# Kernel tuning notes

Hardware: AMD Instinct MI355X
Metric: run time of the kernel (lower is better)

## Reference

```python
import jax, jax.numpy as jnp
import numpy as np

N = 131072      # points (rays x samples chunk)
E = 8           # spatial sub-networks (centroids)
DIN = 90        # encoded pos+dir features fed to sub-NeRFs (xyz_real=True -> x[:, 3:])
H = 256         # sub-NeRF hidden width
DOUT = 4        # rgb + sigma
MARGIN = 2.0    # boundary_margin
EPS = 1e-8


def setup_inputs() -> dict:
    key = jax.random.key(0)
    k = jax.random.split(key, 5)
    x_xyz = jax.random.uniform(k[0], (N, 3), dtype=jnp.float32)          # routing coords in [0,1)^3
    x_feat = jax.random.normal(k[1], (N, DIN), dtype=jnp.float32)        # encoded features
    x = jnp.concatenate([x_xyz, x_feat], axis=1)                         # [N, 3+DIN]
    centroids = jax.random.uniform(k[2], (E, 3), dtype=jnp.float32)
    W1 = jax.random.normal(k[3], (E, DIN, H), dtype=jnp.float32) * 0.05
    b1 = jnp.zeros((E, H), dtype=jnp.float32)
    W2 = jax.random.normal(k[4], (E, H, DOUT), dtype=jnp.float32) * 0.05
    b2 = jnp.zeros((E, DOUT), dtype=jnp.float32)
    return {"x": x, "centroids": centroids, "W1": W1, "b1": b1, "W2": W2, "b2": b2}


def reference(x, centroids, W1, b1, W2, b2):
    # --- centroid routing (torch.cdist equivalent) ---
    xyz = x[:, :3]                                                       # [N,3]
    d2 = jnp.sum((xyz[:, None, :] - centroids[None, :, :]) ** 2, axis=-1)
    dist = jnp.sqrt(jnp.maximum(d2, 0.0))                                # [N,E]
    inv = 1.0 / (dist + EPS)
    min_d = jnp.min(dist, axis=1, keepdims=True)                         # [N,1]
    inv = jnp.where(dist > MARGIN * min_d, 0.0, inv)                     # zero far experts
    weights = inv / jnp.sum(inv, axis=-1, keepdims=True)                 # [N,E], rows sum to 1

    # --- per-expert sub-NeRF MLP, weighted combine ---
    # Dense-equivalent of masked gather + weighted scatter-add: experts whose
    # weight is exactly 0 contribute nothing, matching the torch masked path.
    feat = x[:, 3:]                                                      # xyz_real=True -> drop xyz
    h = jax.nn.relu(jnp.einsum('nd,edh->enh', feat, W1) + b1[:, None, :])  # [E,N,H]
    out_e = jnp.einsum('enh,eho->eno', h, W2) + b2[:, None, :]             # [E,N,DOUT]
    return jnp.einsum('eno,ne->no', out_e, weights)                        # [N,DOUT]
```

## Files before the change

kernel.cpp:

```cpp
#include <hip/hip_runtime.h>

#define NPTS 131072
#define NE 8
#define DIN 90
#define NH 256
#define HPITCH 264

typedef __attribute__((ext_vector_type(8))) short bf16x8;
typedef __attribute__((ext_vector_type(4))) float f32x4;
typedef __attribute__((ext_vector_type(2))) float f32x2;
typedef __attribute__((ext_vector_type(4))) unsigned int u32x4;
typedef __attribute__((ext_vector_type(2))) unsigned int u32x2;
typedef __attribute__((ext_vector_type(4), aligned(4))) float f32x4a;
typedef __attribute__((ext_vector_type(2), aligned(4))) float f32x2a;

__device__ __forceinline__ unsigned short f2bf(float f) {
  unsigned int u = __float_as_uint(f);
  u += 0x7fffu + ((u >> 16) & 1u);
  return (unsigned short)(u >> 16);
}

__device__ __forceinline__ unsigned int pkbf(float f0, float f1) {
  unsigned int u0 = __float_as_uint(f0) + 0x7fffu;
  unsigned int u1 = __float_as_uint(f1) + 0x7fffu;
  return __builtin_amdgcn_perm(u1, u0, 0x07060302u);
}

__device__ __forceinline__ bf16x8 cvt8(f32x4 a, f32x4 b) {
  u32x4 r;
  r[0] = pkbf(a[0], a[1]);
  r[1] = pkbf(a[2], a[3]);
  r[2] = pkbf(b[0], b[1]);
  r[3] = pkbf(b[2], b[3]);
  return __builtin_bit_cast(bf16x8, r);
}

__global__ __launch_bounds__(256) void prep(const float* __restrict__ W1,
                                            const float* __restrict__ W2,
                                            unsigned short* __restrict__ W1T,
                                            unsigned short* __restrict__ W2T) {
  int idx = blockIdx.x * 256 + threadIdx.x;
  const int n1 = NE * NH * 96;
  if (idx < n1) {
    int kp = idx % 96;
    int n  = (idx / 96) % NH;
    int e  = idx / (96 * NH);
    float v = (kp < DIN) ? W1[((size_t)e * DIN + kp) * NH + n] : 0.f;
    W1T[idx] = f2bf(v);
  } else {
    int j = idx - n1;
    if (j < NE * 16 * NH) {
      int k = j % NH;
      int o = (j / NH) % 16;
      int e = j / (16 * NH);
      float v = (o < 4) ? W2[((size_t)e * NH + k) * 4 + o] : 0.f;
      W2T[j] = f2bf(v);
    }
  }
}

__global__ __launch_bounds__(256, 3) void meganerf_main(
    const float* __restrict__ x, const float* __restrict__ cent,
    const float* __restrict__ b1, const float* __restrict__ b2,
    const unsigned short* __restrict__ W1T, const unsigned short* __restrict__ W2T,
    float* __restrict__ out) {
  __shared__ unsigned short sH[64 * HPITCH];
  __shared__ float sW[NE][64];
  __shared__ float sB2[64][4];

  const int t    = threadIdx.x;
  const int lane = t & 63;
  const int wid  = t >> 6;
  const int l15  = lane & 15;
  const int l4   = lane >> 4;
  const int row0 = blockIdx.x * 64;

  bf16x8 bfr[4][3];
#pragma unroll
  for (int nf = 0; nf < 4; ++nf) {
    const float* gr = x + (size_t)(row0 + 16 * nf + l15) * 93 + 3;
    f32x4 v0, v1;
    v0 = *(const f32x4a*)(gr + 8 * l4);
    v1 = *(const f32x4a*)(gr + 8 * l4 + 4);
    bfr[nf][0] = cvt8(v0, v1);
    v0 = *(const f32x4a*)(gr + 32 + 8 * l4);
    v1 = *(const f32x4a*)(gr + 36 + 8 * l4);
    bfr[nf][1] = cvt8(v0, v1);
    if (l4 < 3) {
      v0 = *(const f32x4a*)(gr + 64 + 8 * l4);
      v1 = *(const f32x4a*)(gr + 68 + 8 * l4);
    } else {
      f32x2 tl = *(const f32x2a*)(gr + 88);
      v0[0] = tl[0]; v0[1] = tl[1]; v0[2] = 0.f; v0[3] = 0.f;
      v1[0] = 0.f; v1[1] = 0.f; v1[2] = 0.f; v1[3] = 0.f;
    }
    bfr[nf][2] = cvt8(v0, v1);
  }

  if (t < 64) {
    const float* gx = x + (size_t)(row0 + t) * 93;
    float px = gx[0], py = gx[1], pz = gx[2];
    float dist[NE], inv[NE];
    float mind = 3.4e38f;
#pragma unroll
    for (int e = 0; e < NE; ++e) {
      float dx = px - cent[e * 3 + 0];
      float dy = py - cent[e * 3 + 1];
      float dz = pz - cent[e * 3 + 2];
      float d2 = dx * dx + dy * dy + dz * dz;
      float d = sqrtf(fmaxf(d2, 0.f));
      dist[e] = d;
      inv[e] = 1.f / (d + 1e-8f);
      mind = fminf(mind, d);
    }
    float s = 0.f;
#pragma unroll
    for (int e = 0; e < NE; ++e) {
      if (dist[e] > 2.0f * mind) inv[e] = 0.f;
      s += inv[e];
    }
    float rs = 1.f / s;
    float bb[4] = {0.f, 0.f, 0.f, 0.f};
#pragma unroll
    for (int e = 0; e < NE; ++e) {
      float w = inv[e] * rs;
      sW[e][t] = w;
#pragma unroll
      for (int o = 0; o < 4; ++o) bb[o] += w * b2[e * 4 + o];
    }
#pragma unroll
    for (int o = 0; o < 4; ++o) sB2[t][o] = bb[o];
  }
  __syncthreads();

  f32x4 facc[4] = {{0.f, 0.f, 0.f, 0.f}, {0.f, 0.f, 0.f, 0.f},
                   {0.f, 0.f, 0.f, 0.f}, {0.f, 0.f, 0.f, 0.f}};

  for (int e = 0; e < NE; ++e) {
    float wv[4];
#pragma unroll
    for (int nf = 0; nf < 4; ++nf) wv[nf] = sW[e][16 * nf + l15];

#pragma unroll
    for (int c = 0; c < 2; ++c) {
      const int colbase = 128 * c + 32 * wid;
      f32x4 b1v[2];
#pragma unroll
      for (int mf = 0; mf < 2; ++mf)
        b1v[mf] = *(const f32x4*)(b1 + e * NH + colbase + 16 * mf + 4 * l4);
      f32x4 acc[2][4];
#pragma unroll
      for (int mf = 0; mf < 2; ++mf)
#pragma unroll
        for (int nf = 0; nf < 4; ++nf) acc[mf][nf] = b1v[mf];
#pragma unroll
      for (int ks = 0; ks < 3; ++ks) {
        bf16x8 w1f[2];
#pragma unroll
        for (int mf = 0; mf < 2; ++mf)
          w1f[mf] = *(const bf16x8*)(W1T +
              (size_t)(e * NH + colbase + 16 * mf + l15) * 96 + 32 * ks + 8 * l4);
#pragma unroll
        for (int mf = 0; mf < 2; ++mf)
#pragma unroll
          for (int nf = 0; nf < 4; ++nf)
            acc[mf][nf] = __builtin_amdgcn_mfma_f32_16x16x32_bf16(
                w1f[mf], bfr[nf][ks], acc[mf][nf], 0, 0, 0);
      }
#pragma unroll
      for (int mf = 0; mf < 2; ++mf) {
        const int hcol = colbase + 16 * mf + 4 * l4;
#pragma unroll
        for (int nf = 0; nf < 4; ++nf) {
          const float w = wv[nf];
          f32x4 a = acc[mf][nf];
          f32x2 p0, p1;
          p0[0] = a[0]; p0[1] = a[1];
          p1[0] = a[2]; p1[1] = a[3];
          const f32x2 z = {0.f, 0.f};
          p0 = __builtin_elementwise_max(p0, z) * w;
          p1 = __builtin_elementwise_max(p1, z) * w;
          u32x2 pk;
          pk[0] = pkbf(p0[0], p0[1]);
          pk[1] = pkbf(p1[0], p1[1]);
          *(u32x2*)&sH[(16 * nf + l15) * HPITCH + hcol] = pk;
        }
      }
    }
    __syncthreads();

#pragma unroll
    for (int ks2 = 0; ks2 < 2; ++ks2) {
      const int k = 64 * wid + 32 * ks2 + 8 * l4;
      bf16x8 bw = *(const bf16x8*)(W2T + (size_t)(e * 16 + l15) * NH + k);
#pragma unroll
      for (int rf = 0; rf < 4; ++rf) {
        bf16x8 ah = *(const bf16x8*)&sH[(16 * rf + l15) * HPITCH + k];
        facc[rf] = __builtin_amdgcn_mfma_f32_16x16x32_bf16(ah, bw, facc[rf], 0, 0, 0);
      }
    }
    __syncthreads();
  }

  float* sOutP = (float*)sH;
  if (l15 < 4) {
#pragma unroll
    for (int rf = 0; rf < 4; ++rf)
#pragma unroll
      for (int r = 0; r < 4; ++r)
        sOutP[(wid * 64 + 16 * rf + 4 * l4 + r) * 4 + l15] = facc[rf][r];
  }
  __syncthreads();
  {
    const int row = t >> 2, o = t & 3;
    float v = sB2[row][o] + sOutP[(0 * 64 + row) * 4 + o] + sOutP[(1 * 64 + row) * 4 + o] +
              sOutP[(2 * 64 + row) * 4 + o] + sOutP[(3 * 64 + row) * 4 + o];
    out[row0 * 4 + t] = v;
  }
}

extern "C" void kernel_launch(void* const* d_in, const int* in_sizes, int n_in,
                              void* d_out, int out_size, void* d_ws, size_t ws_size,
                              hipStream_t stream) {
  const float* x    = (const float*)d_in[0];
  const float* cent = (const float*)d_in[1];
  const float* W1   = (const float*)d_in[2];
  const float* b1   = (const float*)d_in[3];
  const float* W2   = (const float*)d_in[4];
  const float* b2   = (const float*)d_in[5];
  float* out = (float*)d_out;

  unsigned short* W1T = (unsigned short*)d_ws;
  unsigned short* W2T = W1T + NE * NH * 96;

  const int prep_total = NE * NH * 96 + NE * 16 * NH;
  prep<<<(prep_total + 255) / 256, 256, 0, stream>>>(W1, W2, W1T, W2T);
  meganerf_main<<<NPTS / 64, 256, 0, stream>>>(x, cent, b1, b2, W1T, W2T, out);
}
```

Baseline: 181.1 us.

## Make hidden tile wave-private to drop per-expert barriers and hoist weight loads

Each wave now writes its slice of the hidden activations into a private shared-memory region, laid out in MFMA fragment order. Each wave then consumes only the K-range it produced in the second GEMM, so the two __syncthreads per expert are removed. W1 and W2 fragments are loaded ahead of the MFMA chains to hide global latency. The prep kernel is rewritten so reads of W1/W2 are coalesced and padding is zero-filled separately. This raises register pressure from the hoisted fragments, which could hurt occupancy at the 3-blocks launch bound.

Measured after the change: 168.1 us. 7.2% less time.

```diff
diff --git a/kernel.cpp b/kernel.cpp
--- a/kernel.cpp
+++ b/kernel.cpp
@@ -4,7 +4,6 @@
 #define NE 8
 #define DIN 90
 #define NH 256
-#define HPITCH 264
 
 typedef __attribute__((ext_vector_type(8))) short bf16x8;
 typedef __attribute__((ext_vector_type(4))) float f32x4;
@@ -35,27 +34,38 @@
   return __builtin_bit_cast(bf16x8, r);
 }
 
+#define PREP_T (184320 + 12288 + 8192 + 24576)
 __global__ __launch_bounds__(256) void prep(const float* __restrict__ W1,
                                             const float* __restrict__ W2,
                                             unsigned short* __restrict__ W1T,
                                             unsigned short* __restrict__ W2T) {
-  int idx = blockIdx.x * 256 + threadIdx.x;
-  const int n1 = NE * NH * 96;
-  if (idx < n1) {
-    int kp = idx % 96;
-    int n  = (idx / 96) % NH;
-    int e  = idx / (96 * NH);
-    float v = (kp < DIN) ? W1[((size_t)e * DIN + kp) * NH + n] : 0.f;
-    W1T[idx] = f2bf(v);
-  } else {
-    int j = idx - n1;
-    if (j < NE * 16 * NH) {
-      int k = j % NH;
-      int o = (j / NH) % 16;
-      int e = j / (16 * NH);
-      float v = (o < 4) ? W2[((size_t)e * NH + k) * 4 + o] : 0.f;
-      W2T[j] = f2bf(v);
-    }
+  int tid = blockIdx.x * 256 + threadIdx.x;
+  if (tid < 184320) {
+    float v = W1[tid];
+    int n = tid & 255, r = tid >> 8;
+    int kp = r % 90, e = r / 90;
+    W1T[(size_t)(e * NH + n) * 96 + kp] = f2bf(v);
+    return;
+  }
+  tid -= 184320;
+  if (tid < 12288) {
+    int kp = 90 + tid % 6, q = tid / 6;
+    int n = q & 255, e = q >> 8;
+    W1T[(size_t)(e * NH + n) * 96 + kp] = 0;
+    return;
+  }
+  tid -= 12288;
+  if (tid < 8192) {
+    float v = W2[tid];
+    int o = tid & 3, k = (tid >> 2) & 255, e = tid >> 10;
+    W2T[(size_t)(e * 16 + o) * NH + k] = f2bf(v);
+    return;
+  }
+  tid -= 8192;
+  if (tid < 24576) {
+    int k = tid & 255, q = tid >> 8;
+    int o = 4 + q % 12, e = q / 12;
+    W2T[(size_t)(e * 16 + o) * NH + k] = 0;
   }
 }
 
@@ -64,7 +74,7 @@
     const float* __restrict__ b1, const float* __restrict__ b2,
     const unsigned short* __restrict__ W1T, const unsigned short* __restrict__ W2T,
     float* __restrict__ out) {
-  __shared__ unsigned short sH[64 * HPITCH];
+  __shared__ unsigned short sH[4 * 4096];
   __shared__ float sW[NE][64];
   __shared__ float sB2[64][4];
 
@@ -74,6 +84,7 @@
   const int l15  = lane & 15;
   const int l4   = lane >> 4;
   const int row0 = blockIdx.x * 64;
+  const int gbase = wid * 4096;
 
   bf16x8 bfr[4][3];
 #pragma unroll
@@ -137,6 +148,11 @@
                    {0.f, 0.f, 0.f, 0.f}, {0.f, 0.f, 0.f, 0.f}};
 
   for (int e = 0; e < NE; ++e) {
+    bf16x8 bw[2];
+#pragma unroll
+    for (int ks2 = 0; ks2 < 2; ++ks2)
+      bw[ks2] = *(const bf16x8*)(W2T + (size_t)(e * 16 + l15) * NH +
+                                 128 * ks2 + 32 * wid + 8 * l4);
     float wv[4];
 #pragma unroll
     for (int nf = 0; nf < 4; ++nf) wv[nf] = sW[e][16 * nf + l15];
@@ -144,6 +160,13 @@
 #pragma unroll
     for (int c = 0; c < 2; ++c) {
       const int colbase = 128 * c + 32 * wid;
+      bf16x8 w1f[2][3];
+#pragma unroll
+      for (int ks = 0; ks < 3; ++ks)
+#pragma unroll
+        for (int mf = 0; mf < 2; ++mf)
+          w1f[mf][ks] = *(const bf16x8*)(W1T +
+              (size_t)(e * NH + colbase + 16 * mf + l15) * 96 + 32 * ks + 8 * l4);
       f32x4 b1v[2];
 #pragma unroll
       for (int mf = 0; mf < 2; ++mf)
@@ -154,22 +177,16 @@
 #pragma unroll
         for (int nf = 0; nf < 4; ++nf) acc[mf][nf] = b1v[mf];
 #pragma unroll
-      for (int ks = 0; ks < 3; ++ks) {
-        bf16x8 w1f[2];
-#pragma unroll
-        for (int mf = 0; mf < 2; ++mf)
-          w1f[mf] = *(const bf16x8*)(W1T +
-              (size_t)(e * NH + colbase + 16 * mf + l15) * 96 + 32 * ks + 8 * l4);
+      for (int ks = 0; ks < 3; ++ks)
 #pragma unroll
         for (int mf = 0; mf < 2; ++mf)
 #pragma unroll
           for (int nf = 0; nf < 4; ++nf)
             acc[mf][nf] = __builtin_amdgcn_mfma_f32_16x16x32_bf16(
-                w1f[mf], bfr[nf][ks], acc[mf][nf], 0, 0, 0);
-      }
+                w1f[mf][ks], bfr[nf][ks], acc[mf][nf], 0, 0, 0);
+
 #pragma unroll
       for (int mf = 0; mf < 2; ++mf) {
-        const int hcol = colbase + 16 * mf + 4 * l4;
 #pragma unroll
         for (int nf = 0; nf < 4; ++nf) {
           const float w = wv[nf];
@@ -183,25 +200,22 @@
           u32x2 pk;
           pk[0] = pkbf(p0[0], p0[1]);
           pk[1] = pkbf(p1[0], p1[1]);
-          *(u32x2*)&sH[(16 * nf + l15) * HPITCH + hcol] = pk;
+          *(u32x2*)&sH[gbase + ((nf * 2 + c) * 64 + (l15 + 16 * (2 * mf + (l4 >> 1)))) * 8 +
+                       4 * (l4 & 1)] = pk;
         }
       }
     }
-    __syncthreads();
-
-#pragma unroll
-    for (int ks2 = 0; ks2 < 2; ++ks2) {
-      const int k = 64 * wid + 32 * ks2 + 8 * l4;
-      bf16x8 bw = *(const bf16x8*)(W2T + (size_t)(e * 16 + l15) * NH + k);
+
+#pragma unroll
+    for (int ks2 = 0; ks2 < 2; ++ks2)
 #pragma unroll
       for (int rf = 0; rf < 4; ++rf) {
-        bf16x8 ah = *(const bf16x8*)&sH[(16 * rf + l15) * HPITCH + k];
-        facc[rf] = __builtin_amdgcn_mfma_f32_16x16x32_bf16(ah, bw, facc[rf], 0, 0, 0);
+        bf16x8 ah = *(const bf16x8*)&sH[gbase + ((rf * 2 + ks2) * 64 + lane) * 8];
+        facc[rf] = __builtin_amdgcn_mfma_f32_16x16x32_bf16(ah, bw[ks2], facc[rf], 0, 0, 0);
       }
-    }
-    __syncthreads();
-  }
-
+  }
+
+  __syncthreads();
   float* sOutP = (float*)sH;
   if (l15 < 4) {
 #pragma unroll
@@ -233,7 +247,6 @@
   unsigned short* W1T = (unsigned short*)d_ws;
   unsigned short* W2T = W1T + NE * NH * 96;
 
-  const int prep_total = NE * NH * 96 + NE * 16 * NH;
-  prep<<<(prep_total + 255) / 256, 256, 0, stream>>>(W1, W2, W1T, W2T);
+  prep<<<(PREP_T + 255) / 256, 256, 0, stream>>>(W1, W2, W1T, W2T);
   meganerf_main<<<NPTS / 64, 256, 0, stream>>>(x, cent, b1, b2, W1T, W2T, out);
 }
```
